# Kernel optimization log

Measured on AMD Instinct MI355X. Metric: run time of the kernel, lower is better.

Reference implementation:

```python
import jax, jax.numpy as jnp
import numpy as np
from jax import lax

N_INPUT = 1024
N_OUTPUT = 1024
B, T = 8, 64


def setup_inputs() -> dict:
    key = jax.random.key(0)
    k1, k2 = jax.random.split(key)
    X = jax.random.normal(k1, (B, T, N_INPUT), dtype=jnp.float32)
    W_init = jax.random.normal(k2, (B, N_OUTPUT, N_INPUT), dtype=jnp.float32) / np.sqrt(N_INPUT)
    return {"X": X, "W_init": W_init}


def reference(X, W_init):
    lr = 1.0 / X.shape[-1]  # self.lr = 1 / n_input

    def step(W, x_t):
        # pre = bmm(W, x_t[...,None]).squeeze(-1)
        pre = jnp.einsum('boi,bi->bo', W, x_t)
        y_t = jax.nn.sigmoid(pre)
        # Oja plasticity rule: dW_ij = y_i * x_j - y_i^2 * W_ij
        dW = jnp.einsum('bo,bi->boi', y_t, x_t) - (y_t ** 2)[..., None] * W
        W_new = W + lr * dW
        return W_new, y_t

    # scan over time (sequential dependency on W)
    _, m_traj = lax.scan(step, W_init, jnp.swapaxes(X, 0, 1))  # [T, B, n_out]
    return jnp.swapaxes(m_traj, 0, 1)  # [B, T, n_out]
```

## Files before the change

### kernel.cpp

```cpp
#include <hip/hip_runtime.h>
#include <hip/hip_bf16.h>


#define BB 8
#define TT 64
#define NI 1024
#define NO 1024

typedef __attribute__((ext_vector_type(8))) short bf16x8;
typedef __attribute__((ext_vector_type(4))) float f32x4;

__device__ __forceinline__ short f2bf(float f) {
    __hip_bfloat16 h = __float2bfloat16(f);
    return __builtin_bit_cast(short, h);
}

__global__ __launch_bounds__(256)
void xcvt_kernel(const float* __restrict__ X, ushort* __restrict__ Xb16)
{
    const int i = blockIdx.x * 256 + threadIdx.x;
    const float4 v = *reinterpret_cast<const float4*>(X + (size_t)i * 4);
    short4 s;
    s.x = f2bf(v.x); s.y = f2bf(v.y); s.z = f2bf(v.z); s.w = f2bf(v.w);
    *reinterpret_cast<short4*>(Xb16 + (size_t)i * 4) = s;
}

__global__ __launch_bounds__(256, 2)
void fused_kernel(const float* __restrict__ W0, const ushort* __restrict__ Xb16,
                  float* __restrict__ out)
{
    __shared__ __align__(16) ushort As[16][520];
    __shared__ __align__(16) float  Gtile[16][68];
    __shared__ __align__(16) float  Sl[64][68];

    const int tid  = threadIdx.x;
    const int lane = tid & 63;
    const int wave = tid >> 6;
    const int b  = blockIdx.x & 7;
    const int nt = blockIdx.x >> 3;
    const int t0 = wave * 16;
    const int r  = lane & 15;
    const int kb = lane >> 4;
    const int j  = tid >> 4;
    const int x  = tid & 15;

    const float* __restrict__ Wrow = W0 + ((size_t)b * NO + nt * 16 + j) * NI;
    float4 v[8];
#pragma unroll
    for (int q = 0; q < 8; ++q)
        v[q] = *reinterpret_cast<const float4*>(Wrow + q * 64 + x * 4);

    bf16x8 breg[32];
    {
        const ushort* __restrict__ Bb =
            Xb16 + ((size_t)b * TT + t0 + r) * NI + kb * 8;
#pragma unroll
        for (int kk = 0; kk < 32; ++kk)
            breg[kk] = *reinterpret_cast<const bf16x8*>(Bb + kk * 32);
    }

#pragma unroll
    for (int q = 0; q < 8; ++q) {
        short4 s4;
        s4.x = f2bf(v[q].x); s4.y = f2bf(v[q].y);
        s4.z = f2bf(v[q].z); s4.w = f2bf(v[q].w);
        *reinterpret_cast<short4*>(&As[j][q * 64 + x * 4]) = s4;
    }
    __syncthreads();

#pragma unroll
    for (int q = 0; q < 8; ++q)
        v[q] = *reinterpret_cast<const float4*>(Wrow + 512 + q * 64 + x * 4);

    f32x4 acc = {0.f, 0.f, 0.f, 0.f};
    const ushort* __restrict__ Ap = &As[r][kb * 8];
#pragma unroll
    for (int kk = 0; kk < 16; ++kk) {
        const bf16x8 a = *reinterpret_cast<const bf16x8*>(Ap + kk * 32);
        acc = __builtin_amdgcn_mfma_f32_16x16x32_bf16(a, breg[kk], acc, 0, 0, 0);
    }
    __syncthreads();

#pragma unroll
    for (int q = 0; q < 8; ++q) {
        short4 s4;
        s4.x = f2bf(v[q].x); s4.y = f2bf(v[q].y);
        s4.z = f2bf(v[q].z); s4.w = f2bf(v[q].w);
        *reinterpret_cast<short4*>(&As[j][q * 64 + x * 4]) = s4;
    }
    __syncthreads();

#pragma unroll
    for (int kk = 0; kk < 16; ++kk) {
        const bf16x8 a = *reinterpret_cast<const bf16x8*>(Ap + kk * 32);
        acc = __builtin_amdgcn_mfma_f32_16x16x32_bf16(a, breg[16 + kk], acc, 0, 0, 0);
    }

    const int tcol = lane & 15;
    const int mrow = (lane >> 4) * 4;
#pragma unroll
    for (int rr = 0; rr < 4; ++rr)
        Gtile[mrow + rr][t0 + tcol] = acc[rr];
    __syncthreads();

#pragma unroll 1
    for (int c = 0; c < 4; ++c) {
        f32x4 sacc = {0.f, 0.f, 0.f, 0.f};
#pragma unroll
        for (int h = 0; h < 2; ++h) {
            const ushort* src =
                Xb16 + ((size_t)b * TT + c * 16 + j) * NI + h * 512 + x * 32;
            *reinterpret_cast<bf16x8*>(&As[j][x * 32])      =
                *reinterpret_cast<const bf16x8*>(src);
            *reinterpret_cast<bf16x8*>(&As[j][x * 32 + 8])  =
                *reinterpret_cast<const bf16x8*>(src + 8);
            *reinterpret_cast<bf16x8*>(&As[j][x * 32 + 16]) =
                *reinterpret_cast<const bf16x8*>(src + 16);
            *reinterpret_cast<bf16x8*>(&As[j][x * 32 + 24]) =
                *reinterpret_cast<const bf16x8*>(src + 24);
            __syncthreads();
#pragma unroll
            for (int kk = 0; kk < 16; ++kk) {
                const bf16x8 a = *reinterpret_cast<const bf16x8*>(Ap + kk * 32);
                sacc = __builtin_amdgcn_mfma_f32_16x16x32_bf16(a, breg[h * 16 + kk],
                                                               sacc, 0, 0, 0);
            }
            __syncthreads();
        }
#pragma unroll
        for (int rr = 0; rr < 4; ++rr)
            Sl[c * 16 + mrow + rr][t0 + tcol] = sacc[rr];
    }
    __syncthreads();

    const int r2 = lane & 3;
    const int jb = lane >> 2;
    const float4 uu = *reinterpret_cast<const float4*>(&Gtile[wave * 4 + r2][jb * 4]);
    float u0 = uu.x, u1 = uu.y, u2 = uu.z, u3 = uu.w;

    const float lr   = 1.0f / 1024.0f;
    const float nL2E = -1.44269504f;
    float y0 = 0.f, y1 = 0.f, y2 = 0.f, y3 = 0.f;

#pragma unroll
    for (int t = 0; t < TT; ++t) {
        const int srcl = (t & 0x3C) | r2;
        const float uv = ((t & 3) == 0) ? u0 : ((t & 3) == 1) ? u1
                       : ((t & 3) == 2) ? u2 : u3;
        const float pre = __shfl(uv, srcl, 64);

        const float e = __builtin_amdgcn_exp2f(pre * nL2E);
        const float y = __builtin_amdgcn_rcpf(1.0f + e);

        const bool own = (jb == (t >> 2));
        if ((t & 3) == 0) y0 = own ? y : y0;
        if ((t & 3) == 1) y1 = own ? y : y1;
        if ((t & 3) == 2) y2 = own ? y : y2;
        if ((t & 3) == 3) y3 = own ? y : y3;

        const float c2 = lr * y;
        const float c1 = fmaf(-c2, y, 1.0f);

        const float4 s = *reinterpret_cast<const float4*>(&Sl[t][jb * 4]);
        u0 = fmaf(c1, u0, c2 * s.x);
        u1 = fmaf(c1, u1, c2 * s.y);
        u2 = fmaf(c1, u2, c2 * s.z);
        u3 = fmaf(c1, u3, c2 * s.w);
    }

    float (*ybuf)[68] = reinterpret_cast<float (*)[68]>(&As[0][0]);
    {
        float4 yv; yv.x = y0; yv.y = y1; yv.z = y2; yv.w = y3;
        *reinterpret_cast<float4*>(&ybuf[wave * 4 + r2][jb * 4]) = yv;
    }
    __syncthreads();

    {
        const int o0 = nt * 16;
        const int t  = tid >> 2;
        const int g  = tid & 3;
        float4 ov;
        ov.x = ybuf[g * 4 + 0][t];
        ov.y = ybuf[g * 4 + 1][t];
        ov.z = ybuf[g * 4 + 2][t];
        ov.w = ybuf[g * 4 + 3][t];
        *reinterpret_cast<float4*>(
            &out[(size_t)b * TT * NO + (size_t)t * NO + o0 + g * 4]) = ov;
    }
}

extern "C" void kernel_launch(void* const* d_in, const int* in_sizes, int n_in,
                              void* d_out, int out_size, void* d_ws, size_t ws_size,
                              hipStream_t stream) {
    const float* X  = (const float*)d_in[0];
    const float* W0 = (const float*)d_in[1];
    float* out = (float*)d_out;

    ushort* Xb16 = (ushort*)d_ws;

    xcvt_kernel<<<512, 256, 0, stream>>>(X, Xb16);
    fused_kernel<<<512, 256, 0, stream>>>(W0, Xb16, out);
}
```

Baseline: 33.58 us.

## Precompute X·Xᵀ Gram matrix once per batch in prep kernel

The per-batch 64x64 Gram matrix of X used by the recurrence was previously recomputed by every one of the 64 blocks of a batch. It is now computed once per batch by 32 extra blocks in the conversion kernel, which convert fp32 X to bf16 on the fly, and written to workspace. The fused kernel then loads it into shared memory, and Gtile now reuses the As buffer. This removes redundant MFMA work and X reloads from the main kernel, at the cost of a global round trip and a slightly longer prep launch.

```diff
diff --git a/kernel.cpp b/kernel.cpp
--- a/kernel.cpp
+++ b/kernel.cpp
@@ -15,22 +15,85 @@
     return __builtin_bit_cast(short, h);
 }
 
-__global__ __launch_bounds__(256)
-void xcvt_kernel(const float* __restrict__ X, ushort* __restrict__ Xb16)
+__global__ __launch_bounds__(256, 2)
+void prep_kernel(const float* __restrict__ X, ushort* __restrict__ Xb16,
+                 float* __restrict__ Sws)
 {
-    const int i = blockIdx.x * 256 + threadIdx.x;
-    const float4 v = *reinterpret_cast<const float4*>(X + (size_t)i * 4);
-    short4 s;
-    s.x = f2bf(v.x); s.y = f2bf(v.y); s.z = f2bf(v.z); s.w = f2bf(v.w);
-    *reinterpret_cast<short4*>(Xb16 + (size_t)i * 4) = s;
+    __shared__ __align__(16) ushort As[16][520];
+
+    const int tid = threadIdx.x;
+    if (blockIdx.x < 512) {
+        const int i = blockIdx.x * 256 + tid;
+        const float4 v = *reinterpret_cast<const float4*>(X + (size_t)i * 4);
+        short4 s;
+        s.x = f2bf(v.x); s.y = f2bf(v.y); s.z = f2bf(v.z); s.w = f2bf(v.w);
+        *reinterpret_cast<short4*>(Xb16 + (size_t)i * 4) = s;
+        return;
+    }
+
+    const int id   = blockIdx.x - 512;
+    const int b    = id & 7;
+    const int c    = id >> 3;
+    const int lane = tid & 63;
+    const int wave = tid >> 6;
+    const int t0 = wave * 16;
+    const int r  = lane & 15;
+    const int kb = lane >> 4;
+    const int j  = tid >> 4;
+    const int x  = tid & 15;
+
+    bf16x8 breg[32];
+    {
+        const float* __restrict__ Bb = X + ((size_t)b * TT + t0 + r) * NI + kb * 8;
+#pragma unroll
+        for (int kk = 0; kk < 32; ++kk) {
+            const float4 lo = *reinterpret_cast<const float4*>(Bb + kk * 32);
+            const float4 hi = *reinterpret_cast<const float4*>(Bb + kk * 32 + 4);
+            bf16x8 f;
+            f[0] = f2bf(lo.x); f[1] = f2bf(lo.y); f[2] = f2bf(lo.z); f[3] = f2bf(lo.w);
+            f[4] = f2bf(hi.x); f[5] = f2bf(hi.y); f[6] = f2bf(hi.z); f[7] = f2bf(hi.w);
+            breg[kk] = f;
+        }
+    }
+
+    const float* __restrict__ Arow = X + ((size_t)b * TT + c * 16 + j) * NI;
+    f32x4 sacc = {0.f, 0.f, 0.f, 0.f};
+    const ushort* __restrict__ Ap = &As[r][kb * 8];
+#pragma unroll
+    for (int h = 0; h < 2; ++h) {
+        float4 v[8];
+#pragma unroll
+        for (int q = 0; q < 8; ++q)
+            v[q] = *reinterpret_cast<const float4*>(Arow + h * 512 + q * 64 + x * 4);
+#pragma unroll
+        for (int q = 0; q < 8; ++q) {
+            short4 s4;
+            s4.x = f2bf(v[q].x); s4.y = f2bf(v[q].y);
+            s4.z = f2bf(v[q].z); s4.w = f2bf(v[q].w);
+            *reinterpret_cast<short4*>(&As[j][q * 64 + x * 4]) = s4;
+        }
+        __syncthreads();
+#pragma unroll
+        for (int kk = 0; kk < 16; ++kk) {
+            const bf16x8 a = *reinterpret_cast<const bf16x8*>(Ap + kk * 32);
+            sacc = __builtin_amdgcn_mfma_f32_16x16x32_bf16(a, breg[h * 16 + kk],
+                                                           sacc, 0, 0, 0);
+        }
+        __syncthreads();
+    }
+
+    const int tcol = lane & 15;
+    const int mrow = (lane >> 4) * 4;
+#pragma unroll
+    for (int rr = 0; rr < 4; ++rr)
+        Sws[((size_t)b * 64 + c * 16 + mrow + rr) * 64 + t0 + tcol] = sacc[rr];
 }
 
 __global__ __launch_bounds__(256, 2)
 void fused_kernel(const float* __restrict__ W0, const ushort* __restrict__ Xb16,
-                  float* __restrict__ out)
+                  const float* __restrict__ Sws, float* __restrict__ out)
 {
     __shared__ __align__(16) ushort As[16][520];
-    __shared__ __align__(16) float  Gtile[16][68];
     __shared__ __align__(16) float  Sl[64][68];
 
     const int tid  = threadIdx.x;
@@ -95,7 +158,9 @@
         const bf16x8 a = *reinterpret_cast<const bf16x8*>(Ap + kk * 32);
         acc = __builtin_amdgcn_mfma_f32_16x16x32_bf16(a, breg[16 + kk], acc, 0, 0, 0);
     }
-
+    __syncthreads();
+
+    float (*Gtile)[68] = reinterpret_cast<float (*)[68]>(&As[0][0]);
     const int tcol = lane & 15;
     const int mrow = (lane >> 4) * 4;
 #pragma unroll
@@ -103,40 +168,23 @@
         Gtile[mrow + rr][t0 + tcol] = acc[rr];
     __syncthreads();
 
-#pragma unroll 1
-    for (int c = 0; c < 4; ++c) {
-        f32x4 sacc = {0.f, 0.f, 0.f, 0.f};
-#pragma unroll
-        for (int h = 0; h < 2; ++h) {
-            const ushort* src =
-                Xb16 + ((size_t)b * TT + c * 16 + j) * NI + h * 512 + x * 32;
-            *reinterpret_cast<bf16x8*>(&As[j][x * 32])      =
-                *reinterpret_cast<const bf16x8*>(src);
-            *reinterpret_cast<bf16x8*>(&As[j][x * 32 + 8])  =
-                *reinterpret_cast<const bf16x8*>(src + 8);
-            *reinterpret_cast<bf16x8*>(&As[j][x * 32 + 16]) =
-                *reinterpret_cast<const bf16x8*>(src + 16);
-            *reinterpret_cast<bf16x8*>(&As[j][x * 32 + 24]) =
-                *reinterpret_cast<const bf16x8*>(src + 24);
-            __syncthreads();
-#pragma unroll
-            for (int kk = 0; kk < 16; ++kk) {
-                const bf16x8 a = *reinterpret_cast<const bf16x8*>(Ap + kk * 32);
-                sacc = __builtin_amdgcn_mfma_f32_16x16x32_bf16(a, breg[h * 16 + kk],
-                                                               sacc, 0, 0, 0);
-            }
-            __syncthreads();
-        }
-#pragma unroll
-        for (int rr = 0; rr < 4; ++rr)
-            Sl[c * 16 + mrow + rr][t0 + tcol] = sacc[rr];
-    }
-    __syncthreads();
+    {
+        const float* __restrict__ Sb = Sws + (size_t)b * 4096;
+#pragma unroll
+        for (int q = 0; q < 4; ++q) {
+            const int idx  = tid + q * 256;
+            const int srow = idx >> 4;
+            const int sx   = idx & 15;
+            *reinterpret_cast<float4*>(&Sl[srow][sx * 4]) =
+                *reinterpret_cast<const float4*>(Sb + srow * 64 + sx * 4);
+        }
+    }
 
     const int r2 = lane & 3;
     const int jb = lane >> 2;
     const float4 uu = *reinterpret_cast<const float4*>(&Gtile[wave * 4 + r2][jb * 4]);
     float u0 = uu.x, u1 = uu.y, u2 = uu.z, u3 = uu.w;
+    __syncthreads();
 
     const float lr   = 1.0f / 1024.0f;
     const float nL2E = -1.44269504f;
@@ -168,7 +216,7 @@
         u3 = fmaf(c1, u3, c2 * s.w);
     }
 
-    float (*ybuf)[68] = reinterpret_cast<float (*)[68]>(&As[0][0]);
+    float (*ybuf)[68] = Gtile;
     {
         float4 yv; yv.x = y0; yv.y = y1; yv.z = y2; yv.w = y3;
         *reinterpret_cast<float4*>(&ybuf[wave * 4 + r2][jb * 4]) = yv;
@@ -196,8 +244,9 @@
     const float* W0 = (const float*)d_in[1];
     float* out = (float*)d_out;
 
-    ushort* Xb16 = (ushort*)d_ws;
-
-    xcvt_kernel<<<512, 256, 0, stream>>>(X, Xb16);
-    fused_kernel<<<512, 256, 0, stream>>>(W0, Xb16, out);
-}
+    float*  Sws  = (float*)d_ws;
+    ushort* Xb16 = (ushort*)((char*)d_ws + 131072);
+
+    prep_kernel<<<544, 256, 0, stream>>>(X, Xb16, Sws);
+    fused_kernel<<<512, 256, 0, stream>>>(W0, Xb16, Sws, out);
+}
```

Measured after the change: 31.88 us. -5.1%, faster.
